# Performance work log

Measured on AMD Instinct MI355X. Metric: run time of the kernel, lower is better.

The kernel has to match this reference:

```python
import jax, jax.numpy as jnp
import numpy as np

B, S, D, NL, H, KV, F, V, R = 4, 1024, 2048, 2, 16, 4, 8192, 32000, 16
HD = D // H                      # 128, Llama-3 head dim
LORA_SCALE = 32.0 / 16.0         # alpha / r
ROPE_THETA = 500000.0
EPS = 1e-5


def _rope_tables(seq_len, hd):
    inv = 1.0 / (ROPE_THETA ** (jnp.arange(0, hd, 2, dtype=jnp.float32) / hd))
    freqs = jnp.arange(seq_len, dtype=jnp.float32)[:, None] * inv[None, :]   # [S, hd/2]
    emb = jnp.concatenate([freqs, freqs], axis=-1)                           # [S, hd]
    return jnp.cos(emb), jnp.sin(emb)


def _apply_rope(x, cos, sin):
    # x: [B, S, nh, HD]; LLaMA rotate_half convention
    h = x.shape[-1] // 2
    rot = jnp.concatenate([-x[..., h:], x[..., :h]], axis=-1)
    return x * cos[None, :, None, :] + rot * sin[None, :, None, :]


def _rmsnorm(x, w):
    return x * jax.lax.rsqrt(jnp.mean(x * x, axis=-1, keepdims=True) + EPS) * w


def _forward(embed, wq, wk, wv, wo, laq, lbq, lav, lbv, wg, wu, wd, n1, n2, nf,
             input_ids, attention_mask):
    b, s = input_ids.shape
    cos, sin = _rope_tables(s, HD)
    amask = attention_mask.astype(bool)
    # causal AND key-padding mask: [B, 1, S, S]
    mask = jnp.tril(jnp.ones((s, s), bool))[None, None] & amask[:, None, None, :]
    x = embed[input_ids]                                   # [B, S, D]
    for l in range(NL):
        h = _rmsnorm(x, n1[l])
        # base projection + LoRA adapter (q and v only, as in target_modules)
        q = h @ wq[l] + ((h @ laq[l].T) @ lbq[l].T) * LORA_SCALE
        k = h @ wk[l]
        v = h @ wv[l] + ((h @ lav[l].T) @ lbv[l].T) * LORA_SCALE
        q = _apply_rope(q.reshape(b, s, H, HD), cos, sin)
        k = _apply_rope(k.reshape(b, s, KV, HD), cos, sin)
        v = v.reshape(b, s, KV, HD)
        k = jnp.repeat(k, H // KV, axis=2)                 # GQA expand
        v = jnp.repeat(v, H // KV, axis=2)
        scores = jnp.einsum('bqhd,bkhd->bhqk', q, k) / jnp.float32(np.sqrt(HD))
        scores = jnp.where(mask, scores, jnp.float32(-1e9))
        attn = jax.nn.softmax(scores, axis=-1)
        o = jnp.einsum('bhqk,bkhd->bqhd', attn, v).reshape(b, s, D)
        x = x + o @ wo[l]
        h2 = _rmsnorm(x, n2[l])
        x = x + (jax.nn.silu(h2 @ wg[l]) * (h2 @ wu[l])) @ wd[l]
    h = _rmsnorm(x, nf)                                    # final norm -> last_hidden_state
    m = attention_mask.astype(jnp.float32)[..., None]
    return (h * m).sum(axis=1) / jnp.clip(m.sum(axis=1), 1e-9)   # masked mean pool [B, D]


def setup_inputs() -> dict:
    key = jax.random.key(0)
    ks = jax.random.split(key, 14)
    sd = 0.02
    nrm = lambda k, shape: sd * jax.random.normal(k, shape, dtype=jnp.float32)
    return {
        'embed': nrm(ks[0], (V, D)),
        'wq': nrm(ks[1], (NL, D, D)),
        'wk': nrm(ks[2], (NL, D, KV * HD)),
        'wv': nrm(ks[3], (NL, D, KV * HD)),
        'wo': nrm(ks[4], (NL, D, D)),
        'laq': nrm(ks[5], (NL, R, D)),
        'lbq': nrm(ks[6], (NL, D, R)),
        'lav': nrm(ks[7], (NL, R, D)),
        'lbv': nrm(ks[8], (NL, KV * HD, R)),
        'wg': nrm(ks[9], (NL, D, F)),
        'wu': nrm(ks[10], (NL, D, F)),
        'wd': nrm(ks[11], (NL, F, D)),
        'n1': jnp.ones((NL, D), jnp.float32),
        'n2': jnp.ones((NL, D), jnp.float32),
        'nf': jnp.ones((D,), jnp.float32),
        'input_ids': jax.random.randint(ks[12], (B, S), 0, V, dtype=jnp.int32),
        'attention_mask': jnp.ones((B, S), jnp.int32),
    }


def reference(embed, wq, wk, wv, wo, laq, lbq, lav, lbv, wg, wu, wd, n1, n2, nf,
              input_ids, attention_mask):
    return _forward(embed, wq, wk, wv, wo, laq, lbq, lav, lbv, wg, wu, wd,
                    n1, n2, nf, input_ids, attention_mask)
```

## Files before the change

### kernel.cpp

```cpp
#include <hip/hip_runtime.h>
#include <math.h>

#define B_  4
#define S_  1024
#define D_  2048
#define NL_ 2
#define H_  16
#define KV_ 4
#define F_  8192
#define R_  16
#define HD_ 128
#define BS_ (B_*S_)
#define QBLK 64
#define KBLK 64

typedef unsigned short u16;
typedef __attribute__((ext_vector_type(8))) __bf16 bf16x8;
typedef __attribute__((ext_vector_type(4))) float  f32x4;

__device__ __forceinline__ u16 f2bf(float f) {
    unsigned x = __float_as_uint(f);
    unsigned r = (x + 0x7fffu + ((x >> 16) & 1u)) >> 16;
    return (u16)r;
}
__device__ __forceinline__ float bf2f(u16 u) {
    return __uint_as_float(((unsigned)u) << 16);
}

__device__ __forceinline__ void gload16(const void* g, void* l) {
    __builtin_amdgcn_global_load_lds((const __attribute__((address_space(1))) void*)g,
                                     (__attribute__((address_space(3))) void*)l, 16, 0, 0);
}

__global__ void embed_kernel(const float* __restrict__ embed,
                             const int* __restrict__ ids,
                             float* __restrict__ x) {
    int tok = blockIdx.x;
    int id  = ids[tok];
    const float4* src = (const float4*)(embed + (size_t)id * D_);
    float4*       dst = (float4*)(x + (size_t)tok * D_);
    for (int i = threadIdx.x; i < D_/4; i += blockDim.x) dst[i] = src[i];
}

template<int OUTBF>
__global__ __launch_bounds__(256) void rmsnorm_kernel(const float* __restrict__ x,
                                                      const float* __restrict__ w,
                                                      void* __restrict__ out) {
    int row = blockIdx.x;
    const float4* xr = (const float4*)(x + (size_t)row * D_);
    float ss = 0.f;
    for (int i = threadIdx.x; i < D_/4; i += 256) {
        float4 v = xr[i];
        ss += v.x*v.x + v.y*v.y + v.z*v.z + v.w*v.w;
    }
    __shared__ float red[4];
    for (int off = 32; off; off >>= 1) ss += __shfl_down(ss, off);
    if ((threadIdx.x & 63) == 0) red[threadIdx.x >> 6] = ss;
    __syncthreads();
    float tot = red[0] + red[1] + red[2] + red[3];
    float scale = rsqrtf(tot / (float)D_ + 1e-5f);
    const float4* w4 = (const float4*)w;
    for (int i = threadIdx.x; i < D_/4; i += 256) {
        float4 v = xr[i], g = w4[i];
        float a = v.x*scale*g.x, b = v.y*scale*g.y, c = v.z*scale*g.z, d = v.w*scale*g.w;
        if (OUTBF) {
            ushort4 o; o.x = f2bf(a); o.y = f2bf(b); o.z = f2bf(c); o.w = f2bf(d);
            ((ushort4*)((u16*)out + (size_t)row * D_))[i] = o;
        } else {
            float4 o; o.x = a; o.y = b; o.z = c; o.w = d;
            ((float4*)((float*)out + (size_t)row * D_))[i] = o;
        }
    }
}

__global__ __launch_bounds__(256) void convt_kernel(const float* __restrict__ in,
                                                    u16* __restrict__ outT,
                                                    int K, int N) {
    __shared__ float tile[32][33];
    int k0 = blockIdx.y * 32, n0 = blockIdx.x * 32;
    int t = threadIdx.x;
    int r = t >> 3, c4 = (t & 7) * 4;
    float4 v = *(const float4*)(in + (size_t)(k0 + r) * N + n0 + c4);
    tile[r][c4] = v.x; tile[r][c4+1] = v.y; tile[r][c4+2] = v.z; tile[r][c4+3] = v.w;
    __syncthreads();
    int n = t >> 3, kc = (t & 7) * 4;
    ushort4 o;
    o.x = f2bf(tile[kc][n]);   o.y = f2bf(tile[kc+1][n]);
    o.z = f2bf(tile[kc+2][n]); o.w = f2bf(tile[kc+3][n]);
    *(ushort4*)(outT + (size_t)(n0 + n) * K + k0 + kc) = o;
}

template<int ACC>
__global__ __launch_bounds__(256) void gemm_bt(const u16* __restrict__ A,
                                               const u16* __restrict__ Bt,
                                               float* __restrict__ C,
                                               int N, int K) {
    __shared__ __align__(16) u16 As[128*64];
    __shared__ __align__(16) u16 Bs[128*64];
    int tid = threadIdx.x, lane = tid & 63;
    int wid = tid >> 6, wm = wid >> 1, wn = wid & 1;
    int m0 = blockIdx.y * 128, n0 = blockIdx.x * 128;
    const u16* Ab = A  + (size_t)m0 * K;
    const u16* Bb = Bt + (size_t)n0 * K;
    f32x4 acc[4][4] = {};
    for (int k0 = 0; k0 < K; k0 += 64) {
        #pragma unroll
        for (int qq = 0; qq < 4; qq++) {
            int u = qq * 256 + tid;
            int row = u >> 3, cu = u & 7, scu = cu ^ (row & 7);
            size_t goff = (size_t)row * K + k0 + scu * 8;
            gload16(Ab + goff, (char*)As + u * 16);
            gload16(Bb + goff, (char*)Bs + u * 16);
        }
        __syncthreads();
        #pragma unroll
        for (int kk = 0; kk < 2; kk++) {
            int cu = kk * 4 + (lane >> 4);
            bf16x8 af[4], bfr[4];
            #pragma unroll
            for (int i = 0; i < 4; i++) {
                int ar = wm * 64 + i * 16 + (lane & 15);
                af[i]  = *(const bf16x8*)((const char*)As + (((ar << 3) | (cu ^ (ar & 7))) << 4));
                int br = wn * 64 + i * 16 + (lane & 15);
                bfr[i] = *(const bf16x8*)((const char*)Bs + (((br << 3) | (cu ^ (br & 7))) << 4));
            }
            #pragma unroll
            for (int i = 0; i < 4; i++)
                #pragma unroll
                for (int j = 0; j < 4; j++)
                    acc[i][j] = __builtin_amdgcn_mfma_f32_16x16x32_bf16(af[i], bfr[j], acc[i][j], 0, 0, 0);
        }
        __syncthreads();
    }
    int r0 = (lane >> 4) * 4, c0 = lane & 15;
    #pragma unroll
    for (int i = 0; i < 4; i++)
        #pragma unroll
        for (int j = 0; j < 4; j++) {
            int row = m0 + wm * 64 + i * 16 + r0;
            int col = n0 + wn * 64 + j * 16 + c0;
            float* cp = C + (size_t)row * N + col;
            #pragma unroll
            for (int r = 0; r < 4; r++) {
                if (ACC) cp[(size_t)r * N] += acc[i][j][r];
                else     cp[(size_t)r * N] = acc[i][j][r];
            }
        }
}

__global__ __launch_bounds__(256) void gemm_gateup_bt(const u16* __restrict__ A,
                                                      const u16* __restrict__ Gt,
                                                      const u16* __restrict__ Ut,
                                                      u16* __restrict__ act,
                                                      int N, int K) {
    __shared__ __align__(16) u16 As[128*64];
    __shared__ __align__(16) u16 Gs[64*64];
    __shared__ __align__(16) u16 Us[64*64];
    int tid = threadIdx.x, lane = tid & 63;
    int wid = tid >> 6, wm = wid >> 1, wn = wid & 1;
    int m0 = blockIdx.y * 128, n0 = blockIdx.x * 64;
    const u16* Ab = A  + (size_t)m0 * K;
    const u16* Gb = Gt + (size_t)n0 * K;
    const u16* Ub = Ut + (size_t)n0 * K;
    f32x4 ag[4][2] = {}, au[4][2] = {};
    for (int k0 = 0; k0 < K; k0 += 64) {
        #pragma unroll
        for (int qq = 0; qq < 4; qq++) {
            int u = qq * 256 + tid;
            int row = u >> 3, cu = u & 7, scu = cu ^ (row & 7);
            gload16(Ab + (size_t)row * K + k0 + scu * 8, (char*)As + u * 16);
        }
        #pragma unroll
        for (int qq = 0; qq < 2; qq++) {
            int u = qq * 256 + tid;
            int row = u >> 3, cu = u & 7, scu = cu ^ (row & 7);
            size_t goff = (size_t)row * K + k0 + scu * 8;
            gload16(Gb + goff, (char*)Gs + u * 16);
            gload16(Ub + goff, (char*)Us + u * 16);
        }
        __syncthreads();
        #pragma unroll
        for (int kk = 0; kk < 2; kk++) {
            int cu = kk * 4 + (lane >> 4);
            bf16x8 af[4], gf[2], uf[2];
            #pragma unroll
            for (int i = 0; i < 4; i++) {
                int ar = wm * 64 + i * 16 + (lane & 15);
                af[i] = *(const bf16x8*)((const char*)As + (((ar << 3) | (cu ^ (ar & 7))) << 4));
            }
            #pragma unroll
            for (int j = 0; j < 2; j++) {
                int br = wn * 32 + j * 16 + (lane & 15);
                int off = ((br << 3) | (cu ^ (br & 7))) << 4;
                gf[j] = *(const bf16x8*)((const char*)Gs + off);
                uf[j] = *(const bf16x8*)((const char*)Us + off);
            }
            #pragma unroll
            for (int i = 0; i < 4; i++)
                #pragma unroll
                for (int j = 0; j < 2; j++) {
                    ag[i][j] = __builtin_amdgcn_mfma_f32_16x16x32_bf16(af[i], gf[j], ag[i][j], 0, 0, 0);
                    au[i][j] = __builtin_amdgcn_mfma_f32_16x16x32_bf16(af[i], uf[j], au[i][j], 0, 0, 0);
                }
        }
        __syncthreads();
    }
    int r0 = (lane >> 4) * 4, c0 = lane & 15;
    #pragma unroll
    for (int i = 0; i < 4; i++)
        #pragma unroll
        for (int j = 0; j < 2; j++) {
            int col = n0 + wn * 32 + j * 16 + c0;
            #pragma unroll
            for (int r = 0; r < 4; r++) {
                int row = m0 + wm * 64 + i * 16 + r0 + r;
                float g = ag[i][j][r], u = au[i][j][r];
                float s = g / (1.f + __expf(-g));
                act[(size_t)row * N + col] = f2bf(s * u);
            }
        }
}

__global__ __launch_bounds__(256) void lora_a_kernel(const u16* __restrict__ h,
                                                     const float* __restrict__ la,
                                                     float* __restrict__ t16) {
    int r = threadIdx.x >> 4;
    int c = threadIdx.x & 15;
    int row = blockIdx.x * 16 + r;
    const ushort4* hr = (const ushort4*)(h + (size_t)row * D_);
    const float4* lr = (const float4*)(la + (size_t)c * D_);
    float acc = 0.f;
    #pragma unroll 4
    for (int i = 0; i < D_/4; i++) {
        ushort4 a = hr[i]; float4 b = lr[i];
        acc += bf2f(a.x)*b.x + bf2f(a.y)*b.y + bf2f(a.z)*b.z + bf2f(a.w)*b.w;
    }
    t16[(size_t)row * R_ + c] = acc;
}

__global__ __launch_bounds__(256) void lora_b_kernel(const float* __restrict__ t16,
                                                     const float* __restrict__ lb,
                                                     float* __restrict__ out, int N) {
    int row = blockIdx.x;
    __shared__ float ts[R_];
    if (threadIdx.x < R_) ts[threadIdx.x] = t16[(size_t)row * R_ + threadIdx.x];
    __syncthreads();
    for (int d = threadIdx.x; d < N; d += 256) {
        const float4* lbr = (const float4*)(lb + (size_t)d * R_);
        float acc = 0.f;
        #pragma unroll
        for (int r4 = 0; r4 < 4; r4++) {
            float4 v = lbr[r4];
            acc += v.x*ts[r4*4] + v.y*ts[r4*4+1] + v.z*ts[r4*4+2] + v.w*ts[r4*4+3];
        }
        out[(size_t)row * N + d] += 2.0f * acc;
    }
}

__global__ void qconv_rope(const float* __restrict__ q, u16* __restrict__ Qc) {
    int tok = blockIdx.x, h = blockIdx.y, t = threadIdx.x;
    int b = tok >> 10, s = tok & (S_ - 1);
    float inv = __expf(-(float)t * (13.122363377404328f / 64.0f));
    float f = (float)s * inv;
    float c = __cosf(f), si = __sinf(f);
    const float* src = q + ((size_t)tok * H_ + h) * HD_;
    float x0 = src[t], x1 = src[t + 64];
    u16* dst = Qc + (((size_t)(b * H_ + h)) * S_ + s) * HD_;
    dst[t]      = f2bf(x0 * c - x1 * si);
    dst[t + 64] = f2bf(x1 * c + x0 * si);
}

__global__ void kconv_rope(const float* __restrict__ k, u16* __restrict__ Kc) {
    int tok = blockIdx.x, h = blockIdx.y, t = threadIdx.x;
    int b = tok >> 10, s = tok & (S_ - 1);
    float inv = __expf(-(float)t * (13.122363377404328f / 64.0f));
    float f = (float)s * inv;
    float c = __cosf(f), si = __sinf(f);
    const float* src = k + ((size_t)tok * KV_ + h) * HD_;
    float x0 = src[t], x1 = src[t + 64];
    u16* dst = Kc + (((size_t)(b * KV_ + h)) * S_ + s) * HD_;
    dst[t]      = f2bf(x0 * c - x1 * si);
    dst[t + 64] = f2bf(x1 * c + x0 * si);
}

__global__ __launch_bounds__(256) void vconv_t(const float* __restrict__ vb,
                                               u16* __restrict__ Vt) {
    __shared__ float tile[32][33];
    int s0 = blockIdx.x * 32, d0 = blockIdx.y * 32;
    int bk = blockIdx.z;
    int b = bk >> 2, kvh = bk & 3;
    int t = threadIdx.x;
    int r = t >> 3, c4 = (t & 7) * 4;
    float4 v = *(const float4*)(vb + (((size_t)(b * S_ + s0 + r)) * KV_ + kvh) * HD_ + d0 + c4);
    tile[r][c4] = v.x; tile[r][c4+1] = v.y; tile[r][c4+2] = v.z; tile[r][c4+3] = v.w;
    __syncthreads();
    int dr = t >> 3, s4 = (t & 7) * 4;
    ushort4 o;
    o.x = f2bf(tile[s4][dr]);   o.y = f2bf(tile[s4+1][dr]);
    o.z = f2bf(tile[s4+2][dr]); o.w = f2bf(tile[s4+3][dr]);
    *(ushort4*)(Vt + (((size_t)(b * KV_ + kvh)) * HD_ + d0 + dr) * S_ + s0 + s4) = o;
}

__global__ __launch_bounds__(256) void flash_attn(const u16* __restrict__ Qc,
                                                  const u16* __restrict__ Kc,
                                                  const u16* __restrict__ Vt,
                                                  const int* __restrict__ am,
                                                  u16* __restrict__ o) {
    __shared__ __align__(16) u16 Ks[64 * 128];
    __shared__ __align__(16) u16 Vs[128 * 64];
    __shared__ __align__(16) u16 Ps[4][16][72];
    __shared__ int am_s[KBLK];
    int qt = blockIdx.x, h = blockIdx.y, b = blockIdx.z;
    int kvh = h >> 2;
    int tid = threadIdx.x, lane = tid & 63, w = tid >> 6;
    int g = lane >> 4, li = lane & 15;

    bf16x8 qf[4];
    const u16* qb = Qc + (((size_t)(b * H_ + h)) * S_ + qt * QBLK + w * 16 + li) * HD_;
    #pragma unroll
    for (int dd = 0; dd < 4; dd++) qf[dd] = *(const bf16x8*)(qb + dd * 32 + g * 8);

    float m_r[4], l_r[4];
    f32x4 oacc[8];
    #pragma unroll
    for (int r = 0; r < 4; r++) { m_r[r] = -1e30f; l_r[r] = 0.f; }
    #pragma unroll
    for (int d = 0; d < 8; d++) oacc[d] = (f32x4){0.f, 0.f, 0.f, 0.f};

    const u16* Kg = Kc + ((size_t)(b * KV_ + kvh)) * S_ * HD_;
    const u16* Vg = Vt + ((size_t)(b * KV_ + kvh)) * HD_ * S_;
    int qg0 = qt * QBLK + w * 16 + g * 4;

    for (int kvt = 0; kvt <= qt; kvt++) {
        int kv0 = kvt * KBLK;
        #pragma unroll
        for (int qq = 0; qq < 4; qq++) {
            int u = qq * 256 + tid;
            int row = u >> 4, p = u & 15;
            gload16(Kg + (size_t)(kv0 + row) * HD_ + (p ^ (row & 7)) * 8, (char*)Ks + u * 16);
        }
        #pragma unroll
        for (int qq = 0; qq < 4; qq++) {
            int u = qq * 256 + tid;
            int row = u >> 3, p = u & 7;
            gload16(Vg + (size_t)row * S_ + kv0 + (p ^ (row & 7)) * 8, (char*)Vs + u * 16);
        }
        if (tid < KBLK) am_s[tid] = am[b * S_ + kv0 + tid];
        __syncthreads();

        float ps[4][4];
        #pragma unroll
        for (int kt = 0; kt < 4; kt++) {
            f32x4 sa = (f32x4){0.f, 0.f, 0.f, 0.f};
            int row = kt * 16 + li;
            #pragma unroll
            for (int dd = 0; dd < 4; dd++) {
                int c = dd * 4 + g;
                bf16x8 kf = *(const bf16x8*)((const char*)Ks + ((row * 16 + (c ^ (row & 7))) << 4));
                sa = __builtin_amdgcn_mfma_f32_16x16x32_bf16(qf[dd], kf, sa, 0, 0, 0);
            }
            int kcol = kv0 + kt * 16 + li;
            int amok = am_s[kt * 16 + li];
            #pragma unroll
            for (int r = 0; r < 4; r++) {
                float s = sa[r] * 0.08838834764831845f;
                ps[kt][r] = (amok && kcol <= qg0 + r) ? s : -1e9f;
            }
        }

        float rmax[4], rsum[4], scl[4];
        #pragma unroll
        for (int r = 0; r < 4; r++)
            rmax[r] = fmaxf(fmaxf(ps[0][r], ps[1][r]), fmaxf(ps[2][r], ps[3][r]));
        #pragma unroll
        for (int msk = 1; msk < 16; msk <<= 1)
            #pragma unroll
            for (int r = 0; r < 4; r++) rmax[r] = fmaxf(rmax[r], __shfl_xor(rmax[r], msk));
        #pragma unroll
        for (int r = 0; r < 4; r++) {
            float mn = fmaxf(m_r[r], rmax[r]);
            scl[r] = __expf(m_r[r] - mn);
            m_r[r] = mn;
            rsum[r] = 0.f;
        }
        #pragma unroll
        for (int kt = 0; kt < 4; kt++)
            #pragma unroll
            for (int r = 0; r < 4; r++) {
                float p = __expf(ps[kt][r] - m_r[r]);
                ps[kt][r] = p;
                rsum[r] += p;
            }
        #pragma unroll
        for (int msk = 1; msk < 16; msk <<= 1)
            #pragma unroll
            for (int r = 0; r < 4; r++) rsum[r] += __shfl_xor(rsum[r], msk);
        #pragma unroll
        for (int r = 0; r < 4; r++) l_r[r] = l_r[r] * scl[r] + rsum[r];
        #pragma unroll
        for (int d = 0; d < 8; d++)
            #pragma unroll
            for (int r = 0; r < 4; r++) oacc[d][r] *= scl[r];

        #pragma unroll
        for (int kt = 0; kt < 4; kt++)
            #pragma unroll
            for (int r = 0; r < 4; r++)
                Ps[w][g * 4 + r][kt * 16 + li] = f2bf(ps[kt][r]);
        __syncthreads();

        bf16x8 pf[2];
        #pragma unroll
        for (int ks = 0; ks < 2; ks++)
            pf[ks] = *(const bf16x8*)&Ps[w][li][ks * 32 + g * 8];
        #pragma unroll
        for (int dblk = 0; dblk < 8; dblk++) {
            int row = dblk * 16 + li;
            #pragma unroll
            for (int ks = 0; ks < 2; ks++) {
                int c = ks * 4 + g;
                bf16x8 vf = *(const bf16x8*)((const char*)Vs + ((row * 8 + (c ^ (row & 7))) << 4));
                oacc[dblk] = __builtin_amdgcn_mfma_f32_16x16x32_bf16(pf[ks], vf, oacc[dblk], 0, 0, 0);
            }
        }
        __syncthreads();
    }

    float invl[4];
    #pragma unroll
    for (int r = 0; r < 4; r++) invl[r] = 1.f / l_r[r];
    #pragma unroll
    for (int dblk = 0; dblk < 8; dblk++)
        #pragma unroll
        for (int r = 0; r < 4; r++) {
            int qrow = qg0 + r;
            o[(((size_t)b * S_ + qrow) * H_ + h) * HD_ + dblk * 16 + li] =
                f2bf(oacc[dblk][r] * invl[r]);
        }
}

__global__ __launch_bounds__(256) void pool_kernel(const float* __restrict__ h,
                                                   const int* __restrict__ am,
                                                   float* __restrict__ out) {
    int b = blockIdx.y;
    int d = blockIdx.x * 256 + threadIdx.x;
    float acc = 0.f, ms = 0.f;
    for (int s = 0; s < S_; s++) {
        float mm = (float)am[b * S_ + s];
        ms  += mm;
        acc += mm * h[((size_t)b * S_ + s) * D_ + d];
    }
    out[(size_t)b * D_ + d] = acc / fmaxf(ms, 1e-9f);
}

extern "C" void kernel_launch(void* const* d_in, const int* in_sizes, int n_in,
                              void* d_out, int out_size, void* d_ws, size_t ws_size,
                              hipStream_t stream) {
    const float* embed = (const float*)d_in[0];
    const float* wq    = (const float*)d_in[1];
    const float* wk    = (const float*)d_in[2];
    const float* wv    = (const float*)d_in[3];
    const float* wo    = (const float*)d_in[4];
    const float* laq   = (const float*)d_in[5];
    const float* lbq   = (const float*)d_in[6];
    const float* lav   = (const float*)d_in[7];
    const float* lbv   = (const float*)d_in[8];
    const float* wg    = (const float*)d_in[9];
    const float* wu    = (const float*)d_in[10];
    const float* wd    = (const float*)d_in[11];
    const float* n1    = (const float*)d_in[12];
    const float* n2    = (const float*)d_in[13];
    const float* nf    = (const float*)d_in[14];
    const int*   ids   = (const int*)d_in[15];
    const int*   am    = (const int*)d_in[16];
    float* out = (float*)d_out;

    char* base = (char*)d_ws;
    float* x   = (float*)base;
    u16*   hbf = (u16*)(base + 33554432);
    u16*   obf = (u16*)(base + 50331648);
    char*  Rg  = base + 67108864;
    float* q   = (float*)Rg;
    float* kb  = (float*)(Rg + 33554432);
    float* vb  = (float*)(Rg + 41943040);
    u16*   act = (u16*)Rg;
    float* hf  = (float*)Rg;
    float* t16 = (float*)(base + 134217728);
    u16*   wT0 = (u16*)(base + 134479872);
    u16*   wT1 = (u16*)(base + 168034304);
    u16*   Qc  = (u16*)(base + 201588736);
    u16*   Kc  = (u16*)(base + 218365952);
    u16*   Vtb = (u16*)(base + 222560256);

    embed_kernel<<<BS_, 256, 0, stream>>>(embed, ids, x);

    for (int l = 0; l < NL_; l++) {
        const float* wql = wq + (size_t)l * D_ * D_;
        const float* wkl = wk + (size_t)l * D_ * (KV_*HD_);
        const float* wvl = wv + (size_t)l * D_ * (KV_*HD_);
        const float* wol = wo + (size_t)l * D_ * D_;
        const float* wgl = wg + (size_t)l * D_ * F_;
        const float* wul = wu + (size_t)l * D_ * F_;
        const float* wdl = wd + (size_t)l * F_ * D_;

        rmsnorm_kernel<1><<<BS_, 256, 0, stream>>>(x, n1 + (size_t)l * D_, hbf);

        convt_kernel<<<dim3(D_/32, D_/32), 256, 0, stream>>>(wql, wT0, D_, D_);
        gemm_bt<0><<<dim3(D_/128, BS_/128), 256, 0, stream>>>(hbf, wT0, q, D_, D_);
        lora_a_kernel<<<BS_/16, 256, 0, stream>>>(hbf, laq + (size_t)l * R_ * D_, t16);
        lora_b_kernel<<<BS_, 256, 0, stream>>>(t16, lbq + (size_t)l * D_ * R_, q, D_);

        convt_kernel<<<dim3((KV_*HD_)/32, D_/32), 256, 0, stream>>>(wkl, wT0, D_, KV_*HD_);
        gemm_bt<0><<<dim3((KV_*HD_)/128, BS_/128), 256, 0, stream>>>(hbf, wT0, kb, KV_*HD_, D_);
        convt_kernel<<<dim3((KV_*HD_)/32, D_/32), 256, 0, stream>>>(wvl, wT0, D_, KV_*HD_);
        gemm_bt<0><<<dim3((KV_*HD_)/128, BS_/128), 256, 0, stream>>>(hbf, wT0, vb, KV_*HD_, D_);
        lora_a_kernel<<<BS_/16, 256, 0, stream>>>(hbf, lav + (size_t)l * R_ * D_, t16);
        lora_b_kernel<<<BS_, 256, 0, stream>>>(t16, lbv + (size_t)l * (KV_*HD_) * R_, vb, KV_*HD_);

        qconv_rope<<<dim3(BS_, H_),  64, 0, stream>>>(q,  Qc);
        kconv_rope<<<dim3(BS_, KV_), 64, 0, stream>>>(kb, Kc);
        vconv_t<<<dim3(S_/32, HD_/32, B_*KV_), 256, 0, stream>>>(vb, Vtb);

        flash_attn<<<dim3(S_/QBLK, H_, B_), 256, 0, stream>>>(Qc, Kc, Vtb, am, obf);

        convt_kernel<<<dim3(D_/32, D_/32), 256, 0, stream>>>(wol, wT0, D_, D_);
        gemm_bt<1><<<dim3(D_/128, BS_/128), 256, 0, stream>>>(obf, wT0, x, D_, D_);

        rmsnorm_kernel<1><<<BS_, 256, 0, stream>>>(x, n2 + (size_t)l * D_, hbf);
        convt_kernel<<<dim3(F_/32, D_/32), 256, 0, stream>>>(wgl, wT0, D_, F_);
        convt_kernel<<<dim3(F_/32, D_/32), 256, 0, stream>>>(wul, wT1, D_, F_);
        gemm_gateup_bt<<<dim3(F_/64, BS_/128), 256, 0, stream>>>(hbf, wT0, wT1, act, F_, D_);
        convt_kernel<<<dim3(D_/32, F_/32), 256, 0, stream>>>(wdl, wT0, F_, D_);
        gemm_bt<1><<<dim3(D_/128, BS_/128), 256, 0, stream>>>(act, wT0, x, D_, F_);
    }

    rmsnorm_kernel<0><<<BS_, 256, 0, stream>>>(x, nf, hf);
    pool_kernel<<<dim3(D_/256, B_), 256, 0, stream>>>(hf, am, out);
}
```

Measured before the change: 2.190 ms.

## Enlarge weight transpose tiles and read K/V directly from global in attention

The fp32-to-bf16 weight transpose now processes 64x64 tiles, four rows per thread, which cuts block count and per-block overhead. Flash attention no longer stages K, V and the mask in shared memory; each wave loads its MFMA fragments directly from global memory, and the block-wide barriers are removed. This trades barrier and LDS-copy cost for redundant global/L2 traffic, since all four waves fetch the same K/V tiles. Dropping the barriers also relies on the per-wave Ps buffer being accessed only by its own wave.

```diff
diff --git a/kernel.cpp b/kernel.cpp
--- a/kernel.cpp
+++ b/kernel.cpp
@@ -76,18 +76,25 @@
 __global__ __launch_bounds__(256) void convt_kernel(const float* __restrict__ in,
                                                     u16* __restrict__ outT,
                                                     int K, int N) {
-    __shared__ float tile[32][33];
-    int k0 = blockIdx.y * 32, n0 = blockIdx.x * 32;
+    __shared__ float tile[64][65];
+    int k0 = blockIdx.y * 64, n0 = blockIdx.x * 64;
     int t = threadIdx.x;
-    int r = t >> 3, c4 = (t & 7) * 4;
-    float4 v = *(const float4*)(in + (size_t)(k0 + r) * N + n0 + c4);
-    tile[r][c4] = v.x; tile[r][c4+1] = v.y; tile[r][c4+2] = v.z; tile[r][c4+3] = v.w;
+    int r = t >> 4, c4 = (t & 15) * 4;
+    #pragma unroll
+    for (int p = 0; p < 4; p++) {
+        float4 v = *(const float4*)(in + (size_t)(k0 + p * 16 + r) * N + n0 + c4);
+        tile[p*16+r][c4]   = v.x; tile[p*16+r][c4+1] = v.y;
+        tile[p*16+r][c4+2] = v.z; tile[p*16+r][c4+3] = v.w;
+    }
     __syncthreads();
-    int n = t >> 3, kc = (t & 7) * 4;
-    ushort4 o;
-    o.x = f2bf(tile[kc][n]);   o.y = f2bf(tile[kc+1][n]);
-    o.z = f2bf(tile[kc+2][n]); o.w = f2bf(tile[kc+3][n]);
-    *(ushort4*)(outT + (size_t)(n0 + n) * K + k0 + kc) = o;
+    #pragma unroll
+    for (int p = 0; p < 4; p++) {
+        int n = p * 16 + r, kc = c4;
+        ushort4 o;
+        o.x = f2bf(tile[kc][n]);   o.y = f2bf(tile[kc+1][n]);
+        o.z = f2bf(tile[kc+2][n]); o.w = f2bf(tile[kc+3][n]);
+        *(ushort4*)(outT + (size_t)(n0 + n) * K + k0 + kc) = o;
+    }
 }
 
 template<int ACC>
@@ -306,10 +313,7 @@
                                                   const u16* __restrict__ Vt,
                                                   const int* __restrict__ am,
                                                   u16* __restrict__ o) {
-    __shared__ __align__(16) u16 Ks[64 * 128];
-    __shared__ __align__(16) u16 Vs[128 * 64];
     __shared__ __align__(16) u16 Ps[4][16][72];
-    __shared__ int am_s[KBLK];
     int qt = blockIdx.x, h = blockIdx.y, b = blockIdx.z;
     int kvh = h >> 2;
     int tid = threadIdx.x, lane = tid & 63, w = tid >> 6;
@@ -329,42 +333,28 @@
 
     const u16* Kg = Kc + ((size_t)(b * KV_ + kvh)) * S_ * HD_;
     const u16* Vg = Vt + ((size_t)(b * KV_ + kvh)) * HD_ * S_;
+    const int* amb = am + b * S_;
     int qg0 = qt * QBLK + w * 16 + g * 4;
 
     for (int kvt = 0; kvt <= qt; kvt++) {
         int kv0 = kvt * KBLK;
-        #pragma unroll
-        for (int qq = 0; qq < 4; qq++) {
-            int u = qq * 256 + tid;
-            int row = u >> 4, p = u & 15;
-            gload16(Kg + (size_t)(kv0 + row) * HD_ + (p ^ (row & 7)) * 8, (char*)Ks + u * 16);
-        }
-        #pragma unroll
-        for (int qq = 0; qq < 4; qq++) {
-            int u = qq * 256 + tid;
-            int row = u >> 3, p = u & 7;
-            gload16(Vg + (size_t)row * S_ + kv0 + (p ^ (row & 7)) * 8, (char*)Vs + u * 16);
-        }
-        if (tid < KBLK) am_s[tid] = am[b * S_ + kv0 + tid];
-        __syncthreads();
 
         float ps[4][4];
         #pragma unroll
         for (int kt = 0; kt < 4; kt++) {
             f32x4 sa = (f32x4){0.f, 0.f, 0.f, 0.f};
-            int row = kt * 16 + li;
+            int krow = kv0 + kt * 16 + li;
+            const u16* kr = Kg + (size_t)krow * HD_;
             #pragma unroll
             for (int dd = 0; dd < 4; dd++) {
-                int c = dd * 4 + g;
-                bf16x8 kf = *(const bf16x8*)((const char*)Ks + ((row * 16 + (c ^ (row & 7))) << 4));
+                bf16x8 kf = *(const bf16x8*)(kr + (dd * 4 + g) * 8);
                 sa = __builtin_amdgcn_mfma_f32_16x16x32_bf16(qf[dd], kf, sa, 0, 0, 0);
             }
-            int kcol = kv0 + kt * 16 + li;
-            int amok = am_s[kt * 16 + li];
+            int amok = amb[krow];
             #pragma unroll
             for (int r = 0; r < 4; r++) {
                 float s = sa[r] * 0.08838834764831845f;
-                ps[kt][r] = (amok && kcol <= qg0 + r) ? s : -1e9f;
+                ps[kt][r] = (amok && krow <= qg0 + r) ? s : -1e9f;
             }
         }
 
@@ -407,23 +397,20 @@
             #pragma unroll
             for (int r = 0; r < 4; r++)
                 Ps[w][g * 4 + r][kt * 16 + li] = f2bf(ps[kt][r]);
-        __syncthreads();
-
         bf16x8 pf[2];
         #pragma unroll
         for (int ks = 0; ks < 2; ks++)
             pf[ks] = *(const bf16x8*)&Ps[w][li][ks * 32 + g * 8];
+
         #pragma unroll
         for (int dblk = 0; dblk < 8; dblk++) {
-            int row = dblk * 16 + li;
+            const u16* vr = Vg + (size_t)(dblk * 16 + li) * S_ + kv0;
             #pragma unroll
             for (int ks = 0; ks < 2; ks++) {
-                int c = ks * 4 + g;
-                bf16x8 vf = *(const bf16x8*)((const char*)Vs + ((row * 8 + (c ^ (row & 7))) << 4));
+                bf16x8 vf = *(const bf16x8*)(vr + (ks * 4 + g) * 8);
                 oacc[dblk] = __builtin_amdgcn_mfma_f32_16x16x32_bf16(pf[ks], vf, oacc[dblk], 0, 0, 0);
             }
         }
-        __syncthreads();
     }
 
     float invl[4];
@@ -505,14 +492,14 @@
 
         rmsnorm_kernel<1><<<BS_, 256, 0, stream>>>(x, n1 + (size_t)l * D_, hbf);
 
-        convt_kernel<<<dim3(D_/32, D_/32), 256, 0, stream>>>(wql, wT0, D_, D_);
+        convt_kernel<<<dim3(D_/64, D_/64), 256, 0, stream>>>(wql, wT0, D_, D_);
         gemm_bt<0><<<dim3(D_/128, BS_/128), 256, 0, stream>>>(hbf, wT0, q, D_, D_);
         lora_a_kernel<<<BS_/16, 256, 0, stream>>>(hbf, laq + (size_t)l * R_ * D_, t16);
         lora_b_kernel<<<BS_, 256, 0, stream>>>(t16, lbq + (size_t)l * D_ * R_, q, D_);
 
-        convt_kernel<<<dim3((KV_*HD_)/32, D_/32), 256, 0, stream>>>(wkl, wT0, D_, KV_*HD_);
+        convt_kernel<<<dim3((KV_*HD_)/64, D_/64), 256, 0, stream>>>(wkl, wT0, D_, KV_*HD_);
         gemm_bt<0><<<dim3((KV_*HD_)/128, BS_/128), 256, 0, stream>>>(hbf, wT0, kb, KV_*HD_, D_);
-        convt_kernel<<<dim3((KV_*HD_)/32, D_/32), 256, 0, stream>>>(wvl, wT0, D_, KV_*HD_);
+        convt_kernel<<<dim3((KV_*HD_)/64, D_/64), 256, 0, stream>>>(wvl, wT0, D_, KV_*HD_);
         gemm_bt<0><<<dim3((KV_*HD_)/128, BS_/128), 256, 0, stream>>>(hbf, wT0, vb, KV_*HD_, D_);
         lora_a_kernel<<<BS_/16, 256, 0, stream>>>(hbf, lav + (size_t)l * R_ * D_, t16);
         lora_b_kernel<<<BS_, 256, 0, stream>>>(t16, lbv + (size_t)l * (KV_*HD_) * R_, vb, KV_*HD_);
@@ -523,14 +510,14 @@
 
         flash_attn<<<dim3(S_/QBLK, H_, B_), 256, 0, stream>>>(Qc, Kc, Vtb, am, obf);
 
-        convt_kernel<<<dim3(D_/32, D_/32), 256, 0, stream>>>(wol, wT0, D_, D_);
+        convt_kernel<<<dim3(D_/64, D_/64), 256, 0, stream>>>(wol, wT0, D_, D_);
         gemm_bt<1><<<dim3(D_/128, BS_/128), 256, 0, stream>>>(obf, wT0, x, D_, D_);
 
         rmsnorm_kernel<1><<<BS_, 256, 0, stream>>>(x, n2 + (size_t)l * D_, hbf);
-        convt_kernel<<<dim3(F_/32, D_/32), 256, 0, stream>>>(wgl, wT0, D_, F_);
-        convt_kernel<<<dim3(F_/32, D_/32), 256, 0, stream>>>(wul, wT1, D_, F_);
+        convt_kernel<<<dim3(F_/64, D_/64), 256, 0, stream>>>(wgl, wT0, D_, F_);
+        convt_kernel<<<dim3(F_/64, D_/64), 256, 0, stream>>>(wul, wT1, D_, F_);
         gemm_gateup_bt<<<dim3(F_/64, BS_/128), 256, 0, stream>>>(hbf, wT0, wT1, act, F_, D_);
-        convt_kernel<<<dim3(D_/32, F_/32), 256, 0, stream>>>(wdl, wT0, F_, D_);
+        convt_kernel<<<dim3(D_/64, F_/64), 256, 0, stream>>>(wdl, wT0, F_, D_);
         gemm_bt<1><<<dim3(D_/128, BS_/128), 256, 0, stream>>>(act, wT0, x, D_, F_);
     }
 
```

New measurement: 2.452 ms. +12.0%, slower.
